# Performance work log

Measured on AMD Instinct MI355X. Metric: run time of the kernel, lower is better.

The kernel has to match this reference:

```python
import jax, jax.numpy as jnp
import numpy as np

B, C, H, W = 16, 256, 64, 64
N = 8                      # num_heads
D = C // N                 # key_dim = head_dim = 32
INIT_VAL, HEADS_RANGE = 1.0, 3.0
SCALING = D ** (-0.5)
EPS = 1e-6


def _rel_pos(h, w):
    # RetNetRelPos2d, chunkwise_recurrent=True branch
    ang = 1.0 / 10000 ** jnp.linspace(0.0, 1.0, D // 2)
    ang = jnp.repeat(ang, 2)                                   # [D]
    idx = jnp.arange(h * w, dtype=jnp.float32)
    sin = jnp.sin(idx[:, None] * ang[None, :]).reshape(h, w, D)
    cos = jnp.cos(idx[:, None] * ang[None, :]).reshape(h, w, D)
    decay = jnp.log(1.0 - 2.0 ** (-INIT_VAL - HEADS_RANGE * jnp.arange(N, dtype=jnp.float32) / N))
    def d1(l):
        i = jnp.arange(l, dtype=jnp.float32)
        return jnp.abs(i[:, None] - i[None, :]) * decay[:, None, None]   # [N,l,l]
    return sin, cos, d1(h), d1(w)


def _rotate_every_two(x):
    x1 = x[..., ::2]
    x2 = x[..., 1::2]
    return jnp.stack([-x2, x1], axis=-1).reshape(x.shape)


def _theta_shift(x, sin, cos):
    return x * cos + _rotate_every_two(x) * sin


def _layernorm(x, g, b):
    m = jnp.mean(x, axis=-1, keepdims=True)
    v = jnp.mean((x - m) ** 2, axis=-1, keepdims=True)
    return g * (x - m) * jax.lax.rsqrt(v + EPS) + b


def setup_inputs() -> dict:
    key = jax.random.key(0)
    ks = jax.random.split(key, 8)
    s = 0.02
    def w(k, shape):
        return (jax.random.normal(k, shape, jnp.float32) * s)
    return {
        "x": jax.random.normal(ks[0], (B, C, H, W), jnp.float32),
        "Wq": w(ks[1], (C, C)), "bq": jnp.zeros((C,), jnp.float32),
        "Wk": w(ks[2], (C, C)), "bk": jnp.zeros((C,), jnp.float32),
        "Wv": w(ks[3], (C, C)), "bv": jnp.zeros((C,), jnp.float32),
        "lepe_w": w(ks[4], (5, 5, 1, C)), "lepe_b": jnp.zeros((C,), jnp.float32),
        "Wo": w(ks[5], (C, C)), "bo": jnp.zeros((C,), jnp.float32),
        "Wfc": w(ks[6], (C, C)), "bfc": jnp.zeros((C,), jnp.float32),
        "g1": jnp.ones((C,), jnp.float32), "b1": jnp.zeros((C,), jnp.float32),
        "g2": jnp.ones((C,), jnp.float32), "b2": jnp.zeros((C,), jnp.float32),
    }


def _vrc(x, sin, cos, mask_h, mask_w, Wq, bq, Wk, bk, Wv, bv, lepe_w, lepe_b, Wo, bo):
    # x: [B,H,W,C]
    b, h, w, _ = x.shape
    q = x @ Wq + bq
    k = (x @ Wk + bk) * SCALING
    v = x @ Wv + bv
    # lepe: depthwise 5x5 conv on v (NHWC)
    lepe = jax.lax.conv_general_dilated(
        v, lepe_w, window_strides=(1, 1), padding=((2, 2), (2, 2)),
        dimension_numbers=("NHWC", "HWIO", "NHWC"), feature_group_count=C) + lepe_b
    # [B,N,H,W,D]
    q = q.reshape(b, h, w, N, D).transpose(0, 3, 1, 2, 4)
    k = k.reshape(b, h, w, N, D).transpose(0, 3, 1, 2, 4)
    qr = _theta_shift(q, sin, cos)
    kr = _theta_shift(k, sin, cos)
    # ---- W-axis attention: [B,H,N,W,W] ----
    qr_w = qr.transpose(0, 2, 1, 3, 4)           # [B,H,N,W,D]
    kr_w = kr.transpose(0, 2, 1, 3, 4)
    v5 = v.reshape(b, h, w, N, D).transpose(0, 1, 3, 2, 4)   # [B,H,N,W,D]
    qk_w = jnp.einsum("bhnqd,bhnkd->bhnqk", qr_w, kr_w) + mask_w
    v5 = jnp.einsum("bhnqk,bhnkd->bhnqd", jax.nn.softmax(qk_w, axis=-1), v5)
    # ---- H-axis attention: [B,W,N,H,H] ----
    qr_h = qr.transpose(0, 3, 1, 2, 4)           # [B,W,N,H,D]
    kr_h = kr.transpose(0, 3, 1, 2, 4)
    v6 = v5.transpose(0, 3, 2, 1, 4)             # [B,W,N,H,D]
    qk_h = jnp.einsum("bwnqd,bwnkd->bwnqk", qr_h, kr_h) + mask_h
    out = jnp.einsum("bwnqk,bwnkd->bwnqd", jax.nn.softmax(qk_h, axis=-1), v6)
    out = out.transpose(0, 3, 1, 2, 4).reshape(b, h, w, C)   # [B,H,W,C]
    return (out + lepe) @ Wo + bo


def reference(x, Wq, bq, Wk, bk, Wv, bv, lepe_w, lepe_b, Wo, bo, Wfc, bfc, g1, b1, g2, b2):
    xt = x.transpose(0, 2, 3, 1)                 # [B,H,W,C]
    sin, cos, mask_h, mask_w = _rel_pos(H, W)
    y = _vrc(xt, sin, cos, mask_h, mask_w, Wq, bq, Wk, bk, Wv, bv, lepe_w, lepe_b, Wo, bo)
    xt = _layernorm(xt + y, g1, b1)
    xt = _layernorm(xt + (xt @ Wfc + bfc), g2, b2)
    return xt.transpose(0, 3, 1, 2)              # [B,C,H,W]
```

## Files before the change

### kernel.cpp

```cpp
#include <hip/hip_runtime.h>
#include <math.h>

#define B_ 16
#define C_ 256
#define N_ 8
#define D_ 32
#define M_ (B_*64*64)
#define SCALING 0.17677669529663687f

typedef short  bf16x8 __attribute__((ext_vector_type(8)));
typedef float  f32x4  __attribute__((ext_vector_type(4)));
typedef unsigned short u16x8 __attribute__((ext_vector_type(8)));

__device__ __forceinline__ unsigned short f2bf(float f) {
    unsigned u = __float_as_uint(f);
    u += 0x7fffu + ((u >> 16) & 1u);
    return (unsigned short)(u >> 16);
}
__device__ __forceinline__ float bf2f(unsigned short h) {
    return __uint_as_float(((unsigned)h) << 16);
}
__device__ __forceinline__ void gld16(const void* g, void* l) {
    __builtin_amdgcn_global_load_lds(
        (const __attribute__((address_space(1))) unsigned*)g,
        (__attribute__((address_space(3))) unsigned*)l, 16, 0, 0);
}

__global__ __launch_bounds__(256) void k_tables(float* __restrict__ sint_t,
                                                float* __restrict__ cost_t,
                                                float* __restrict__ maskt)
{
    int t = blockIdx.x * 256 + threadIdx.x;
    int d = t >> 12, p = t & 4095;
    int j = d >> 1;
    float ang = (float)pow(10000.0, -(double)j / 15.0);
    float arg = (float)p * ang;
    sint_t[t] = sinf(arg);
    cost_t[t] = cosf(arg);
    if (t < N_*64*64) {
        int n = t >> 12;
        int q = (t >> 6) & 63, k = t & 63;
        int ad = (q > k) ? (q - k) : (k - q);
        double decay = log(1.0 - exp2(-1.0 - 3.0 * (double)n / 8.0));
        maskt[t] = (float)((double)ad * decay);
    }
}

__global__ __launch_bounds__(256) void k_wcvt(
    const float* __restrict__ Wq, const float* __restrict__ Wk,
    const float* __restrict__ Wv, const float* __restrict__ Wo,
    const float* __restrict__ Wfc,
    unsigned short* __restrict__ Wqt, unsigned short* __restrict__ Wkt,
    unsigned short* __restrict__ Wvt, unsigned short* __restrict__ Wot,
    unsigned short* __restrict__ Wfct)
{
    __shared__ float t[32][33];
    int z = blockIdx.z;
    const float* W = z==0?Wq : z==1?Wk : z==2?Wv : z==3?Wo : Wfc;
    unsigned short* Wt = z==0?Wqt : z==1?Wkt : z==2?Wvt : z==3?Wot : Wfct;
    float sc = (z==1) ? SCALING : 1.0f;
    int tx = threadIdx.x & 31, ty = threadIdx.x >> 5;
    int bx = blockIdx.x * 32;
    int by = blockIdx.y * 32;
    #pragma unroll
    for (int j = 0; j < 4; ++j)
        t[ty + j*8][tx] = W[(by + ty + j*8) * 256 + bx + tx];
    __syncthreads();
    #pragma unroll
    for (int j = 0; j < 4; ++j)
        Wt[(bx + ty + j*8) * 256 + by + tx] = f2bf(t[tx][ty + j*8] * sc);
}

__global__ __launch_bounds__(256) void k_prep(const float* __restrict__ x,
                                              float* __restrict__ xt,
                                              unsigned short* __restrict__ xbf)
{
    __shared__ float t[32][33];
    int tx = threadIdx.x & 31, ty = threadIdx.x >> 5;
    int bx = blockIdx.x * 32;
    int by = blockIdx.y * 32;
    size_t bo = (size_t)blockIdx.z * (256*4096);
    #pragma unroll
    for (int j = 0; j < 4; ++j)
        t[ty + j*8][tx] = x[bo + (size_t)(by + ty + j*8) * 4096 + bx + tx];
    __syncthreads();
    #pragma unroll
    for (int j = 0; j < 4; ++j) {
        float v = t[tx][ty + j*8];
        size_t o = bo + (size_t)(bx + ty + j*8) * 256 + by + tx;
        xt[o] = v;
        xbf[o] = f2bf(v);
    }
}

__device__ __forceinline__ void mfma128(
    const unsigned short* A, const unsigned short* Bt, int r0, int c0,
    unsigned short* As, unsigned short* Bs, f32x4 acc[4][4])
{
    const int tid = threadIdx.x;
    const int w = tid >> 6, l = tid & 63;
    const int wr = w >> 1, wc = w & 1;
    const int fr = l & 15, fq = l >> 4;
    const int srow = 32*w + (l >> 2);
    const int skel = (l & 3) * 8;
    for (int kt = 0; kt < 256; kt += 32) {
        __syncthreads();
        gld16(A  + (size_t)(r0 + srow)      * 256 + kt + skel, As + (32*w)    * 32);
        gld16(A  + (size_t)(r0 + srow + 16) * 256 + kt + skel, As + (32*w+16) * 32);
        gld16(Bt + (size_t)(c0 + srow)      * 256 + kt + skel, Bs + (32*w)    * 32);
        gld16(Bt + (size_t)(c0 + srow + 16) * 256 + kt + skel, Bs + (32*w+16) * 32);
        __syncthreads();
        bf16x8 af[4], bfr[4];
        #pragma unroll
        for (int i = 0; i < 4; ++i)
            af[i] = *(const bf16x8*)(As + (wr*64 + i*16 + fr)*32 + fq*8);
        #pragma unroll
        for (int j = 0; j < 4; ++j)
            bfr[j] = *(const bf16x8*)(Bs + (wc*64 + j*16 + fr)*32 + fq*8);
        #pragma unroll
        for (int i = 0; i < 4; ++i)
            #pragma unroll
            for (int j = 0; j < 4; ++j)
                acc[i][j] = __builtin_amdgcn_mfma_f32_16x16x32_bf16(
                    af[i], bfr[j], acc[i][j], 0, 0, 0);
    }
}

__global__ __launch_bounds__(256) void k_qkv(
    const unsigned short* __restrict__ xbf,
    const unsigned short* __restrict__ Wqt, const unsigned short* __restrict__ Wkt,
    const unsigned short* __restrict__ Wvt,
    const float* __restrict__ bq, const float* __restrict__ bk,
    const float* __restrict__ bv,
    unsigned short* __restrict__ qb, unsigned short* __restrict__ kb,
    unsigned short* __restrict__ vb,
    const float* __restrict__ sint_t, const float* __restrict__ cost_t)
{
    __shared__ __align__(16) unsigned short As[4096], Bs[4096];
    int z = blockIdx.z;
    const unsigned short* Bt = z==0?Wqt : z==1?Wkt : Wvt;
    const float* bias = z==0?bq : z==1?bk : bv;
    unsigned short* dst = z==0?qb : z==1?kb : vb;
    int r0 = blockIdx.x * 128, c0 = blockIdx.y * 128;

    f32x4 acc[4][4];
    #pragma unroll
    for (int i = 0; i < 4; ++i)
        #pragma unroll
        for (int j = 0; j < 4; ++j) { f32x4 zr = {0.f,0.f,0.f,0.f}; acc[i][j] = zr; }
    mfma128(xbf, Bt, r0, c0, As, Bs, acc);

    int l = threadIdx.x & 63, w = threadIdx.x >> 6;
    int wr = w>>1, wc = w&1, fr = l&15, fq = l>>4;
    #pragma unroll
    for (int j = 0; j < 4; ++j) {
        int c = c0 + wc*64 + j*16 + fr;
        float bval = bias[c] * (z==1 ? SCALING : 1.0f);
        int n = c >> 5, dl = c & 31;
        #pragma unroll
        for (int i = 0; i < 4; ++i) {
            int rbase = r0 + wr*64 + i*16 + fq*4;
            int b = rbase >> 12;
            int pos0 = rbase & 4095;
            f32x4 v = acc[i][j];
            v[0] += bval; v[1] += bval; v[2] += bval; v[3] += bval;
            if (z < 2) {
                float4 s4 = *(const float4*)(sint_t + dl*4096 + pos0);
                float4 c4 = *(const float4*)(cost_t + dl*4096 + pos0);
                float p0 = __shfl_xor(v[0], 1);
                float p1 = __shfl_xor(v[1], 1);
                float p2 = __shfl_xor(v[2], 1);
                float p3 = __shfl_xor(v[3], 1);
                if (fr & 1) {
                    v[0] = v[0]*c4.x + p0*s4.x;  v[1] = v[1]*c4.y + p1*s4.y;
                    v[2] = v[2]*c4.z + p2*s4.z;  v[3] = v[3]*c4.w + p3*s4.w;
                } else {
                    v[0] = v[0]*c4.x - p0*s4.x;  v[1] = v[1]*c4.y - p1*s4.y;
                    v[2] = v[2]*c4.z - p2*s4.z;  v[3] = v[3]*c4.w - p3*s4.w;
                }
            }
            size_t obase = (size_t)(b*8 + n) * 131072;
            #pragma unroll
            for (int rg = 0; rg < 4; ++rg)
                dst[obase + (size_t)(pos0 + rg)*32 + dl] = f2bf(v[rg]);
        }
    }
}

__global__ __launch_bounds__(256) void k_gemm_bf(
    const unsigned short* __restrict__ A, const unsigned short* __restrict__ Bt,
    const float* __restrict__ bias, float* __restrict__ out)
{
    __shared__ __align__(16) unsigned short As[4096], Bs[4096];
    int r0 = blockIdx.x * 128, c0 = blockIdx.y * 128;
    f32x4 acc[4][4];
    #pragma unroll
    for (int i = 0; i < 4; ++i)
        #pragma unroll
        for (int j = 0; j < 4; ++j) { f32x4 zr = {0.f,0.f,0.f,0.f}; acc[i][j] = zr; }
    mfma128(A, Bt, r0, c0, As, Bs, acc);
    int l = threadIdx.x & 63, w = threadIdx.x >> 6;
    int wr = w>>1, wc = w&1, fr = l&15, fq = l>>4;
    #pragma unroll
    for (int j = 0; j < 4; ++j) {
        int c = c0 + wc*64 + j*16 + fr;
        float bval = bias[c];
        #pragma unroll
        for (int i = 0; i < 4; ++i) {
            int rbase = r0 + wr*64 + i*16 + fq*4;
            #pragma unroll
            for (int rg = 0; rg < 4; ++rg)
                out[(size_t)(rbase + rg)*256 + c] = acc[i][j][rg] + bval;
        }
    }
}

__global__ __launch_bounds__(256) void k_conv(
    const unsigned short* __restrict__ v, const float* __restrict__ cw,
    const float* __restrict__ cb, float* __restrict__ out)
{
    __shared__ float vs[5*68*36];
    __shared__ float wts[25*32];
    int h = blockIdx.x, n = blockIdx.y, b = blockIdx.z;
    int tid = threadIdx.x;
    for (int i = tid; i < 5*68*36; i += 256) vs[i] = 0.f;
    for (int i = tid; i < 800; i += 256) {
        int tap = i >> 5, d = i & 31;
        wts[i] = cw[tap*256 + n*32 + d];
    }
    __syncthreads();
    const unsigned short* vb_ = v + (size_t)((b*8 + n)*64) * 2048;
    #pragma unroll
    for (int it = 0; it < 5; ++it) {
        int f  = tid + it*256;
        int rr = f >> 8;
        int f2 = f & 255;
        int w  = f2 >> 2, d8 = (f2 & 3) * 8;
        int hh = h + rr - 2;
        if (hh >= 0 && hh < 64) {
            u16x8 vv = *(const u16x8*)(vb_ + hh*2048 + w*32 + d8);
            float* dp = vs + (rr*68 + w + 2)*36 + d8;
            #pragma unroll
            for (int e = 0; e < 8; ++e) dp[e] = bf2f(vv[e]);
        }
    }
    __syncthreads();
    int d = tid & 31, wq = tid >> 5;
    float wreg[25];
    #pragma unroll
    for (int t5 = 0; t5 < 25; ++t5) wreg[t5] = wts[t5*32 + d];
    float bias = cb[n*32 + d];
    for (int w = wq; w < 64; w += 8) {
        float acc = bias;
        #pragma unroll
        for (int dy = 0; dy < 5; ++dy)
            #pragma unroll
            for (int dx = 0; dx < 5; ++dx)
                acc = fmaf(vs[(dy*68 + w + dx)*36 + d], wreg[dy*5+dx], acc);
        out[(size_t)((b*64 + h)*64 + w)*256 + n*32 + d] = acc;
    }
}

__global__ __launch_bounds__(256) void k_attn(
    const unsigned short* __restrict__ Qb, const unsigned short* __restrict__ Kb,
    const unsigned short* Vb, const float* __restrict__ maskt,
    const float* __restrict__ lepe, unsigned short* Ob, int dir)
{
    __shared__ float Qs[64*36];
    __shared__ float Ks[64*36];
    __shared__ float Vs[64*36];
    __shared__ float Ps[64*68];
    int gid = blockIdx.x;
    int tid = threadIdx.x;
    int n = (gid >> 6) & 7;
    int base, sstr;
    if (dir == 0) { base = gid * 2048;                              sstr = 32;   }
    else          { base = (gid >> 6) * 131072 + (gid & 63) * 32;   sstr = 2048; }

    {
        int s  = tid >> 2;
        int d8 = (tid & 3) * 8;
        size_t ga = (size_t)base + (size_t)s*sstr + d8;
        int la = s*36 + d8;
        u16x8 qv = *(const u16x8*)(Qb + ga);
        u16x8 kv = *(const u16x8*)(Kb + ga);
        u16x8 vv = *(const u16x8*)(Vb + ga);
        #pragma unroll
        for (int e = 0; e < 8; ++e) {
            Qs[la+e] = bf2f(qv[e]);
            Ks[la+e] = bf2f(kv[e]);
            Vs[la+e] = bf2f(vv[e]);
        }
    }
    __syncthreads();

    int q = tid >> 2, kl = tid & 3;
    float4 qreg[8];
    #pragma unroll
    for (int j = 0; j < 8; ++j) qreg[j] = *(const float4*)(Qs + q*36 + j*4);
    float sv[16];
    const float* mrow = maskt + n*4096 + q*64;
    #pragma unroll
    for (int i = 0; i < 16; ++i) {
        int k = kl + i*4;
        const float4* krow = (const float4*)(Ks + k*36);
        float s = 0.f;
        #pragma unroll
        for (int j = 0; j < 8; ++j) {
            float4 kv = krow[j];
            s = fmaf(qreg[j].x, kv.x, s);
            s = fmaf(qreg[j].y, kv.y, s);
            s = fmaf(qreg[j].z, kv.z, s);
            s = fmaf(qreg[j].w, kv.w, s);
        }
        sv[i] = s + mrow[k];
    }
    float m = sv[0];
    #pragma unroll
    for (int i = 1; i < 16; ++i) m = fmaxf(m, sv[i]);
    m = fmaxf(m, __shfl_xor(m, 1, 4));
    m = fmaxf(m, __shfl_xor(m, 2, 4));
    float sum = 0.f;
    #pragma unroll
    for (int i = 0; i < 16; ++i) { sv[i] = __expf(sv[i] - m); sum += sv[i]; }
    sum += __shfl_xor(sum, 1, 4);
    sum += __shfl_xor(sum, 2, 4);
    float rinv = 1.f / sum;
    #pragma unroll
    for (int i = 0; i < 16; ++i) Ps[q*68 + kl + i*4] = sv[i] * rinv;
    __syncthreads();

    int d0 = (tid & 3) * 8;
    float o[8] = {0,0,0,0,0,0,0,0};
    for (int k = 0; k < 64; ++k) {
        float p = Ps[q*68 + k];
        float4 va  = *(const float4*)(Vs + k*36 + d0);
        float4 vb2 = *(const float4*)(Vs + k*36 + d0 + 4);
        o[0]=fmaf(p,va.x,o[0]);  o[1]=fmaf(p,va.y,o[1]);
        o[2]=fmaf(p,va.z,o[2]);  o[3]=fmaf(p,va.w,o[3]);
        o[4]=fmaf(p,vb2.x,o[4]); o[5]=fmaf(p,vb2.y,o[5]);
        o[6]=fmaf(p,vb2.z,o[6]); o[7]=fmaf(p,vb2.w,o[7]);
    }
    if (dir == 0) {
        u16x8 ov;
        #pragma unroll
        for (int e = 0; e < 8; ++e) ov[e] = f2bf(o[e]);
        *(u16x8*)(Ob + (size_t)base + q*32 + d0) = ov;
    } else {
        int b = gid >> 9, w2 = gid & 63;
        size_t lrow = ((size_t)(b*64 + q)*64 + w2)*256 + n*32 + d0;
        float4 l0 = *(const float4*)(lepe + lrow);
        float4 l1 = *(const float4*)(lepe + lrow + 4);
        o[0]+=l0.x; o[1]+=l0.y; o[2]+=l0.z; o[3]+=l0.w;
        o[4]+=l1.x; o[5]+=l1.y; o[6]+=l1.z; o[7]+=l1.w;
        u16x8 ov;
        #pragma unroll
        for (int e = 0; e < 8; ++e) ov[e] = f2bf(o[e]);
        *(u16x8*)(Ob + lrow) = ov;
    }
}

template<bool BFOUT>
__global__ __launch_bounds__(256) void k_ln(
    const float* A, const float* __restrict__ Bv,
    const float* __restrict__ g, const float* __restrict__ bb,
    float* out, unsigned short* __restrict__ outbf)
{
    int row  = blockIdx.x * 4 + (threadIdx.x >> 6);
    int lane = threadIdx.x & 63;
    size_t off = (size_t)row * 256 + lane*4;
    float4 a4 = *(const float4*)(A + off);
    float4 b4 = *(const float4*)(Bv + off);
    float v0=a4.x+b4.x, v1=a4.y+b4.y, v2=a4.z+b4.z, v3=a4.w+b4.w;
    float s = v0+v1+v2+v3;
    #pragma unroll
    for (int mm = 1; mm < 64; mm <<= 1) s += __shfl_xor(s, mm, 64);
    float mean = s * (1.0f/256.0f);
    float d0=v0-mean, d1=v1-mean, d2=v2-mean, d3=v3-mean;
    float qq = d0*d0 + d1*d1 + d2*d2 + d3*d3;
    #pragma unroll
    for (int mm = 1; mm < 64; mm <<= 1) qq += __shfl_xor(qq, mm, 64);
    float rstd = rsqrtf(qq * (1.0f/256.0f) + 1e-6f);
    float4 g4  = *(const float4*)(g + lane*4);
    float4 be4 = *(const float4*)(bb + lane*4);
    float o0 = g4.x*d0*rstd + be4.x, o1 = g4.y*d1*rstd + be4.y;
    float o2 = g4.z*d2*rstd + be4.z, o3 = g4.w*d3*rstd + be4.w;
    *(float4*)(out + off) = make_float4(o0, o1, o2, o3);
    if (BFOUT) {
        ushort4 ov = make_ushort4(f2bf(o0), f2bf(o1), f2bf(o2), f2bf(o3));
        *(ushort4*)(outbf + off) = ov;
    }
}

__global__ __launch_bounds__(256) void k_transpose(const float* __restrict__ src,
                                                   float* __restrict__ dst,
                                                   int rows, int cols)
{
    __shared__ float t[32][33];
    int tx = threadIdx.x & 31, ty = threadIdx.x >> 5;
    int bx = blockIdx.x * 32, by = blockIdx.y * 32;
    size_t bo = (size_t)blockIdx.z * rows * cols;
    #pragma unroll
    for (int j = 0; j < 4; ++j)
        t[ty + j*8][tx] = src[bo + (size_t)(by + ty + j*8) * cols + bx + tx];
    __syncthreads();
    #pragma unroll
    for (int j = 0; j < 4; ++j)
        dst[bo + (size_t)(bx + ty + j*8) * rows + by + tx] = t[tx][ty + j*8];
}

extern "C" void kernel_launch(void* const* d_in, const int* in_sizes, int n_in,
                              void* d_out, int out_size, void* d_ws, size_t ws_size,
                              hipStream_t stream)
{
    (void)in_sizes; (void)n_in; (void)out_size;
    const float* x   = (const float*)d_in[0];
    const float* Wq  = (const float*)d_in[1];
    const float* bq  = (const float*)d_in[2];
    const float* Wk  = (const float*)d_in[3];
    const float* bk  = (const float*)d_in[4];
    const float* Wv  = (const float*)d_in[5];
    const float* bv  = (const float*)d_in[6];
    const float* lw  = (const float*)d_in[7];
    const float* lb  = (const float*)d_in[8];
    const float* Wo  = (const float*)d_in[9];
    const float* bo  = (const float*)d_in[10];
    const float* Wfc = (const float*)d_in[11];
    const float* bfc = (const float*)d_in[12];
    const float* g1  = (const float*)d_in[13];
    const float* b1  = (const float*)d_in[14];
    const float* g2  = (const float*)d_in[15];
    const float* b2  = (const float*)d_in[16];
    float* out = (float*)d_out;

    const size_t NBB = 67108864;
    const size_t NEED = 3*NBB + 2*524288 + 131072 + 5*131072;
    if (ws_size < NEED) return;

    char* wsb = (char*)d_ws;
    float*          xt   = (float*)wsb;
    unsigned short* xbf  = (unsigned short*)(wsb + NBB);
    unsigned short* qb   = (unsigned short*)(wsb + NBB + NBB/2);
    unsigned short* kb   = (unsigned short*)(wsb + 2*NBB);
    unsigned short* vb   = (unsigned short*)(wsb + 2*NBB + NBB/2);
    float*          yb   = (float*)(wsb + NBB + NBB/2);
    float* sint_t = (float*)(wsb + 3*NBB);
    float* cost_t = sint_t + 131072;
    float* maskt  = cost_t + 131072;
    unsigned short* Wqt  = (unsigned short*)(maskt + 32768);
    unsigned short* Wkt  = Wqt + 65536;
    unsigned short* Wvt  = Wkt + 65536;
    unsigned short* Wot  = Wvt + 65536;
    unsigned short* Wfct = Wot + 65536;

    k_tables<<<512, 256, 0, stream>>>(sint_t, cost_t, maskt);
    k_wcvt<<<dim3(8,8,5), 256, 0, stream>>>(Wq,Wk,Wv,Wo,Wfc,
                                            Wqt,Wkt,Wvt,Wot,Wfct);
    k_prep<<<dim3(128,8,16), 256, 0, stream>>>(x, xt, xbf);
    k_qkv<<<dim3(512,2,3), 256, 0, stream>>>(xbf, Wqt,Wkt,Wvt, bq,bk,bv,
                                             qb,kb,vb, sint_t,cost_t);
    k_conv<<<dim3(64,8,16), 256, 0, stream>>>(vb, lw, lb, out);
    k_attn<<<8192, 256, 0, stream>>>(qb, kb, vb, maskt, nullptr, vb, 0);
    k_attn<<<8192, 256, 0, stream>>>(qb, kb, vb, maskt, out, xbf, 1);
    k_gemm_bf<<<dim3(512,2), 256, 0, stream>>>(xbf, Wot, bo, yb);
    k_ln<true><<<16384, 256, 0, stream>>>(xt, yb, g1, b1, xt, xbf);
    k_gemm_bf<<<dim3(512,2), 256, 0, stream>>>(xbf, Wfct, bfc, out);
    k_ln<false><<<16384, 256, 0, stream>>>(xt, out, g2, b2, yb, nullptr);
    k_transpose<<<dim3(8,128,16), 256, 0, stream>>>(yb, out, 4096, 256);
}
```

Baseline: 602.5 us.

## Rewrite axial attention with bf16 MFMA, one wave per sequence, inline decay mask

Replaces the scalar fp32 axial attention kernel with an MFMA version in which each wavefront handles one 64-length sequence. QK^T and PV use 16x16x32 bf16 matrix instructions, and the softmax stays in registers with row reductions done by lane shuffles. The decay mask is computed inline from |q-k|*decay instead of being read from a precomputed table, so the mask table and its setup code are removed. P is now rounded to bf16 before the PV product, and normalisation is deferred to the output, which adds some numerical error. Output stores change from 16-byte vectors to scalar 2-byte writes, which may reduce store efficiency in the strided direction.

```diff
diff --git a/kernel.cpp b/kernel.cpp
--- a/kernel.cpp
+++ b/kernel.cpp
@@ -27,8 +27,7 @@
 }
 
 __global__ __launch_bounds__(256) void k_tables(float* __restrict__ sint_t,
-                                                float* __restrict__ cost_t,
-                                                float* __restrict__ maskt)
+                                                float* __restrict__ cost_t)
 {
     int t = blockIdx.x * 256 + threadIdx.x;
     int d = t >> 12, p = t & 4095;
@@ -37,13 +36,6 @@
     float arg = (float)p * ang;
     sint_t[t] = sinf(arg);
     cost_t[t] = cosf(arg);
-    if (t < N_*64*64) {
-        int n = t >> 12;
-        int q = (t >> 6) & 63, k = t & 63;
-        int ad = (q > k) ? (q - k) : (k - q);
-        double decay = log(1.0 - exp2(-1.0 - 3.0 * (double)n / 8.0));
-        maskt[t] = (float)((double)ad * decay);
-    }
 }
 
 __global__ __launch_bounds__(256) void k_wcvt(
@@ -261,102 +253,123 @@
     }
 }
 
-__global__ __launch_bounds__(256) void k_attn(
+__global__ __launch_bounds__(256, 3) void k_attn_mfma(
     const unsigned short* __restrict__ Qb, const unsigned short* __restrict__ Kb,
-    const unsigned short* Vb, const float* __restrict__ maskt,
-    const float* __restrict__ lepe, unsigned short* Ob, int dir)
-{
-    __shared__ float Qs[64*36];
-    __shared__ float Ks[64*36];
-    __shared__ float Vs[64*36];
-    __shared__ float Ps[64*68];
-    int gid = blockIdx.x;
+    const unsigned short* Vb, const float* __restrict__ lepe,
+    unsigned short* Ob, int dir)
+{
+    __shared__ unsigned short S[4 * 4864];
     int tid = threadIdx.x;
+    int wv = tid >> 6, l = tid & 63;
+    int gid = blockIdx.x * 4 + wv;
     int n = (gid >> 6) & 7;
-    int base, sstr;
-    if (dir == 0) { base = gid * 2048;                              sstr = 32;   }
-    else          { base = (gid >> 6) * 131072 + (gid & 63) * 32;   sstr = 2048; }
-
-    {
-        int s  = tid >> 2;
-        int d8 = (tid & 3) * 8;
-        size_t ga = (size_t)base + (size_t)s*sstr + d8;
-        int la = s*36 + d8;
-        u16x8 qv = *(const u16x8*)(Qb + ga);
-        u16x8 kv = *(const u16x8*)(Kb + ga);
-        u16x8 vv = *(const u16x8*)(Vb + ga);
-        #pragma unroll
-        for (int e = 0; e < 8; ++e) {
-            Qs[la+e] = bf2f(qv[e]);
-            Ks[la+e] = bf2f(kv[e]);
-            Vs[la+e] = bf2f(vv[e]);
-        }
-    }
-    __syncthreads();
-
-    int q = tid >> 2, kl = tid & 3;
-    float4 qreg[8];
-    #pragma unroll
-    for (int j = 0; j < 8; ++j) qreg[j] = *(const float4*)(Qs + q*36 + j*4);
-    float sv[16];
-    const float* mrow = maskt + n*4096 + q*64;
-    #pragma unroll
-    for (int i = 0; i < 16; ++i) {
-        int k = kl + i*4;
-        const float4* krow = (const float4*)(Ks + k*36);
-        float s = 0.f;
-        #pragma unroll
-        for (int j = 0; j < 8; ++j) {
-            float4 kv = krow[j];
-            s = fmaf(qreg[j].x, kv.x, s);
-            s = fmaf(qreg[j].y, kv.y, s);
-            s = fmaf(qreg[j].z, kv.z, s);
-            s = fmaf(qreg[j].w, kv.w, s);
-        }
-        sv[i] = s + mrow[k];
-    }
-    float m = sv[0];
-    #pragma unroll
-    for (int i = 1; i < 16; ++i) m = fmaxf(m, sv[i]);
-    m = fmaxf(m, __shfl_xor(m, 1, 4));
-    m = fmaxf(m, __shfl_xor(m, 2, 4));
-    float sum = 0.f;
-    #pragma unroll
-    for (int i = 0; i < 16; ++i) { sv[i] = __expf(sv[i] - m); sum += sv[i]; }
-    sum += __shfl_xor(sum, 1, 4);
-    sum += __shfl_xor(sum, 2, 4);
-    float rinv = 1.f / sum;
-    #pragma unroll
-    for (int i = 0; i < 16; ++i) Ps[q*68 + kl + i*4] = sv[i] * rinv;
-    __syncthreads();
-
-    int d0 = (tid & 3) * 8;
-    float o[8] = {0,0,0,0,0,0,0,0};
-    for (int k = 0; k < 64; ++k) {
-        float p = Ps[q*68 + k];
-        float4 va  = *(const float4*)(Vs + k*36 + d0);
-        float4 vb2 = *(const float4*)(Vs + k*36 + d0 + 4);
-        o[0]=fmaf(p,va.x,o[0]);  o[1]=fmaf(p,va.y,o[1]);
-        o[2]=fmaf(p,va.z,o[2]);  o[3]=fmaf(p,va.w,o[3]);
-        o[4]=fmaf(p,vb2.x,o[4]); o[5]=fmaf(p,vb2.y,o[5]);
-        o[6]=fmaf(p,vb2.z,o[6]); o[7]=fmaf(p,vb2.w,o[7]);
-    }
-    if (dir == 0) {
-        u16x8 ov;
-        #pragma unroll
-        for (int e = 0; e < 8; ++e) ov[e] = f2bf(o[e]);
-        *(u16x8*)(Ob + (size_t)base + q*32 + d0) = ov;
-    } else {
-        int b = gid >> 9, w2 = gid & 63;
-        size_t lrow = ((size_t)(b*64 + q)*64 + w2)*256 + n*32 + d0;
-        float4 l0 = *(const float4*)(lepe + lrow);
-        float4 l1 = *(const float4*)(lepe + lrow + 4);
-        o[0]+=l0.x; o[1]+=l0.y; o[2]+=l0.z; o[3]+=l0.w;
-        o[4]+=l1.x; o[5]+=l1.y; o[6]+=l1.z; o[7]+=l1.w;
-        u16x8 ov;
-        #pragma unroll
-        for (int e = 0; e < 8; ++e) ov[e] = f2bf(o[e]);
-        *(u16x8*)(Ob + lrow) = ov;
+    int c = l & 15, g = l >> 4;
+    size_t base; int sstr;
+    if (dir == 0) { base = (size_t)gid * 2048;                               sstr = 32;   }
+    else          { base = (size_t)(gid >> 6) * 131072 + (size_t)(gid & 63) * 32; sstr = 2048; }
+
+    unsigned short* Vt = S + wv * 4864;
+    unsigned short* Ps = Vt + 2304;
+
+    float decayf = (float)log(1.0 - exp2(-1.0 - 3.0 * (double)n / 8.0));
+
+    #pragma unroll
+    for (int it = 0; it < 4; ++it) {
+        u16x8 vv = *(const u16x8*)(Vb + base + (size_t)l * sstr + it*8);
+        #pragma unroll
+        for (int e = 0; e < 8; ++e)
+            Vt[(it*8 + e)*72 + l] = vv[e];
+    }
+
+    bf16x8 qf[4], kf[4];
+    #pragma unroll
+    for (int i = 0; i < 4; ++i) {
+        qf[i] = *(const bf16x8*)(Qb + base + (size_t)(i*16 + c) * sstr + g*8);
+        kf[i] = *(const bf16x8*)(Kb + base + (size_t)(i*16 + c) * sstr + g*8);
+    }
+
+    f32x4 acc[4][4];
+    #pragma unroll
+    for (int i = 0; i < 4; ++i)
+        #pragma unroll
+        for (int j = 0; j < 4; ++j) { f32x4 zr = {0.f,0.f,0.f,0.f}; acc[i][j] = zr; }
+    #pragma unroll
+    for (int i = 0; i < 4; ++i)
+        #pragma unroll
+        for (int j = 0; j < 4; ++j)
+            acc[i][j] = __builtin_amdgcn_mfma_f32_16x16x32_bf16(
+                qf[i], kf[j], acc[i][j], 0, 0, 0);
+
+    float rinv[4][4];
+    #pragma unroll
+    for (int i = 0; i < 4; ++i) {
+        #pragma unroll
+        for (int r = 0; r < 4; ++r) {
+            float qi = (float)(i*16 + g*4 + r);
+            float m = -1e30f;
+            #pragma unroll
+            for (int j = 0; j < 4; ++j) {
+                float ki = (float)(j*16 + c);
+                acc[i][j][r] += fabsf(qi - ki) * decayf;
+                m = fmaxf(m, acc[i][j][r]);
+            }
+            m = fmaxf(m, __shfl_xor(m, 1, 16));
+            m = fmaxf(m, __shfl_xor(m, 2, 16));
+            m = fmaxf(m, __shfl_xor(m, 4, 16));
+            m = fmaxf(m, __shfl_xor(m, 8, 16));
+            float s = 0.f;
+            #pragma unroll
+            for (int j = 0; j < 4; ++j) {
+                float e = __expf(acc[i][j][r] - m);
+                acc[i][j][r] = e;
+                s += e;
+            }
+            s += __shfl_xor(s, 1, 16);
+            s += __shfl_xor(s, 2, 16);
+            s += __shfl_xor(s, 4, 16);
+            s += __shfl_xor(s, 8, 16);
+            rinv[i][r] = 1.f / s;
+        }
+    }
+
+    f32x4 o[4][2];
+    #pragma unroll
+    for (int i = 0; i < 4; ++i) { f32x4 zr = {0.f,0.f,0.f,0.f}; o[i][0] = zr; o[i][1] = zr; }
+    #pragma unroll
+    for (int s = 0; s < 2; ++s) {
+        #pragma unroll
+        for (int i = 0; i < 4; ++i)
+            #pragma unroll
+            for (int r = 0; r < 4; ++r)
+                #pragma unroll
+                for (int jj = 0; jj < 2; ++jj)
+                    Ps[(i*16 + g*4 + r)*40 + jj*16 + c] = f2bf(acc[i][2*s + jj][r]);
+        bf16x8 vf0 = *(const bf16x8*)(Vt + (     c)*72 + s*32 + g*8);
+        bf16x8 vf1 = *(const bf16x8*)(Vt + (16 + c)*72 + s*32 + g*8);
+        #pragma unroll
+        for (int i = 0; i < 4; ++i) {
+            bf16x8 pa = *(const bf16x8*)(Ps + (i*16 + c)*40 + g*8);
+            o[i][0] = __builtin_amdgcn_mfma_f32_16x16x32_bf16(pa, vf0, o[i][0], 0, 0, 0);
+            o[i][1] = __builtin_amdgcn_mfma_f32_16x16x32_bf16(pa, vf1, o[i][1], 0, 0, 0);
+        }
+    }
+
+    #pragma unroll
+    for (int i = 0; i < 4; ++i) {
+        #pragma unroll
+        for (int r = 0; r < 4; ++r) {
+            int q = i*16 + g*4 + r;
+            float ri = rinv[i][r];
+            if (dir == 0) {
+                Ob[base + (size_t)q*32 + c]      = f2bf(o[i][0][r] * ri);
+                Ob[base + (size_t)q*32 + 16 + c] = f2bf(o[i][1][r] * ri);
+            } else {
+                int b = gid >> 9, w2 = gid & 63;
+                size_t idx = ((size_t)((b*64 + q)*64 + w2))*256 + n*32 + c;
+                Ob[idx]      = f2bf(o[i][0][r] * ri + lepe[idx]);
+                Ob[idx + 16] = f2bf(o[i][1][r] * ri + lepe[idx + 16]);
+            }
+        }
     }
 }
 
@@ -434,7 +447,7 @@
     float* out = (float*)d_out;
 
     const size_t NBB = 67108864;
-    const size_t NEED = 3*NBB + 2*524288 + 131072 + 5*131072;
+    const size_t NEED = 3*NBB + 2*524288 + 5*131072;
     if (ws_size < NEED) return;
 
     char* wsb = (char*)d_ws;
@@ -446,22 +459,21 @@
     float*          yb   = (float*)(wsb + NBB + NBB/2);
     float* sint_t = (float*)(wsb + 3*NBB);
     float* cost_t = sint_t + 131072;
-    float* maskt  = cost_t + 131072;
-    unsigned short* Wqt  = (unsigned short*)(maskt + 32768);
+    unsigned short* Wqt  = (unsigned short*)(cost_t + 131072);
     unsigned short* Wkt  = Wqt + 65536;
     unsigned short* Wvt  = Wkt + 65536;
     unsigned short* Wot  = Wvt + 65536;
     unsigned short* Wfct = Wot + 65536;
 
-    k_tables<<<512, 256, 0, stream>>>(sint_t, cost_t, maskt);
+    k_tables<<<512, 256, 0, stream>>>(sint_t, cost_t);
     k_wcvt<<<dim3(8,8,5), 256, 0, stream>>>(Wq,Wk,Wv,Wo,Wfc,
                                             Wqt,Wkt,Wvt,Wot,Wfct);
     k_prep<<<dim3(128,8,16), 256, 0, stream>>>(x, xt, xbf);
     k_qkv<<<dim3(512,2,3), 256, 0, stream>>>(xbf, Wqt,Wkt,Wvt, bq,bk,bv,
                                              qb,kb,vb, sint_t,cost_t);
     k_conv<<<dim3(64,8,16), 256, 0, stream>>>(vb, lw, lb, out);
-    k_attn<<<8192, 256, 0, stream>>>(qb, kb, vb, maskt, nullptr, vb, 0);
-    k_attn<<<8192, 256, 0, stream>>>(qb, kb, vb, maskt, out, xbf, 1);
+    k_attn_mfma<<<2048, 256, 0, stream>>>(qb, kb, vb, nullptr, vb, 0);
+    k_attn_mfma<<<2048, 256, 0, stream>>>(qb, kb, vb, out, xbf, 1);
     k_gemm_bf<<<dim3(512,2), 256, 0, stream>>>(xbf, Wot, bo, yb);
     k_ln<true><<<16384, 256, 0, stream>>>(xt, yb, g1, b1, xt, xbf);
     k_gemm_bf<<<dim3(512,2), 256, 0, stream>>>(xbf, Wfct, bfc, out);
```

After: 514.7 us. 14.6% less time.
